# Performance work log

Hardware: AMD Instinct MI355X
Metric: run time of the kernel (lower is better)

The kernel has to match this reference:

```python
import jax, jax.numpy as jnp
import numpy as np

V = 6890  # SMPL vertex count
E = 41328  # directed edges of SMPL mesh
B = 32


def conv1x1(x, W, b):
    # Conv1d kernel=1: pointwise channel mix. x: [B,C,L], W: [O,C], b: [O]
    return jnp.einsum('bcl,oc->bol', x, W) + b[None, :, None]


def setup_inputs() -> dict:
    key = jax.random.key(0)
    ks = jax.random.split(key, 24)
    w = lambda k, s: jax.random.normal(k, s, jnp.float32) * 0.02
    img_feat = jax.random.normal(ks[0], (B, 720, 56, 56), jnp.float32)
    # symmetric random edge list standing in for the fixed SMPL mesh edges
    src = jax.random.randint(ks[1], (E // 2,), 0, V)
    dst = jax.random.randint(ks[2], (E // 2,), 0, V)
    edge_index = jnp.concatenate([jnp.stack([src, dst]), jnp.stack([dst, src])], axis=1).astype(jnp.int32)
    return {
        'img_feat': img_feat,
        'edge_index': edge_index,
        'Wx': w(ks[3], (V, 720)), 'bx': w(ks[4], (V,)),
        'Wy': w(ks[5], (V, 720)), 'by': w(ks[6], (V,)),
        'Wz1': w(ks[7], (56 * 224, 720)), 'bz1': w(ks[8], (56 * 224,)),
        'Wz2': w(ks[9], (V, 224)), 'bz2': w(ks[10], (V,)),
        'Ww1': w(ks[11], (56 * 224, 720)), 'bw1': w(ks[12], (56 * 224,)),
        'Ww2': w(ks[13], (V, 224)), 'bw2': w(ks[14], (V,)),
        'Wg1': w(ks[15], (168, 64)), 'bg1': w(ks[16], (64,)),
        'Wg2': w(ks[17], (64, 32)), 'bg2': w(ks[18], (32,)),
        'Wg3': w(ks[19], (32, 3)), 'bg3': w(ks[20], (3,)),
    }


def reference(img_feat, edge_index, Wx, bx, Wy, by, Wz1, bz1, Wz2, bz2,
              Ww1, bw1, Ww2, bw2, Wg1, bg1, Wg2, bg2, Wg3, bg3):
    b = img_feat.shape[0]
    # 1x1 conv heatmap heads
    heatmap_x = conv1x1(img_feat.mean(2), Wx, bx)            # [B,V,56]
    heatmap_y = conv1x1(img_feat.mean(3), Wy, by)            # [B,V,56]
    feat_g = img_feat.mean((2, 3))[:, :, None]               # [B,720,1]
    heatmap_z = conv1x1(conv1x1(feat_g, Wz1, bz1).reshape(b, 224, 56), Wz2, bz2)
    heatmap_w = conv1x1(conv1x1(feat_g, Ww1, bw1).reshape(b, 224, 56), Ww2, bw2)
    coord_w = jax.nn.sigmoid(heatmap_w.mean(-1, keepdims=True))  # [B,V,1]
    xyz = jnp.concatenate([heatmap_x, heatmap_y, heatmap_z], -1)  # [B,V,168]

    # GCN normalization with self-loops (PyG gcn_norm, edge_weight=1)
    loops = jnp.arange(V, dtype=edge_index.dtype)
    src = jnp.concatenate([edge_index[0], loops])
    dst = jnp.concatenate([edge_index[1], loops])
    deg = jnp.zeros((V,), xyz.dtype).at[dst].add(1.0)
    dinv = jnp.where(deg > 0, jax.lax.rsqrt(deg), 0.0)
    norm = dinv[src] * dinv[dst]                              # [E+V]

    def gcn(x, W, bias):
        xw = x @ W                                            # [B,V,out]
        msg = xw[:, src, :] * norm[None, :, None]             # gather + scale
        agg = jnp.zeros((b, V, W.shape[1]), x.dtype).at[:, dst, :].add(msg)
        return agg + bias

    h = jax.nn.leaky_relu(gcn(xyz, Wg1, bg1))
    h = jax.nn.leaky_relu(gcn(h, Wg2, bg2))
    h = gcn(h, Wg3, bg3)                                      # [B,V,3]
    return jnp.concatenate([h, coord_w], 2)                   # [B,V,4]
```

## Files before the change

### kernel.cpp

```cpp
#include <hip/hip_runtime.h>
#include <hip/hip_bf16.h>
#include <math.h>

#define NV 6890
#define BATCH 32
#define C720 720
#define HW 56
#define K2 1792
#define NBIG 2048
#define MPAD 6912

typedef __attribute__((ext_vector_type(8))) short bf16x8;
typedef __attribute__((ext_vector_type(4))) float f32x4;

__device__ inline void gload16(const void* g, void* l) {
  __builtin_amdgcn_global_load_lds((const __attribute__((address_space(1))) void*)g,
                                   (__attribute__((address_space(3))) void*)l, 16, 0, 0);
}
__device__ inline float bf2f(short s) {
  union { unsigned u; float f; } c; c.u = ((unsigned)(unsigned short)s) << 16; return c.f;
}
__device__ inline short f2bf(float f) {
  __hip_bfloat16 h = (__hip_bfloat16)f; return *(short*)&h;
}

__global__ __launch_bounds__(256) void k_misc(
    const float* __restrict__ Wg1, const float* __restrict__ Ww1, const float* __restrict__ bw1,
    float* __restrict__ S, float* __restrict__ Mw1, float* __restrict__ mb1,
    int* __restrict__ deg) {
  const int blk = blockIdx.x, tid = threadIdx.x;
  if (blk < 672) {
    int c = blk / 3, chunk = blk - c * 3;
    if (tid < 240) {
      int k = chunk * 240 + tid;
      float s = 0.f;
      for (int l = 0; l < HW; ++l) s += Ww1[(size_t)(c * HW + l) * 720 + k];
      Mw1[c * 720 + k] = s * (1.f / HW);
    }
    return;
  }
  if (tid < 64) {
    float s0 = 0, s1 = 0, s2 = 0;
    for (int l = 0; l < HW; ++l) {
      s0 += Wg1[l * 64 + tid];
      s1 += Wg1[(HW + l) * 64 + tid];
      s2 += Wg1[(112 + l) * 64 + tid];
    }
    S[tid] = s0; S[64 + tid] = s1; S[128 + tid] = s2;
  }
  if (tid < 224) {
    float s = 0.f;
    for (int l = 0; l < HW; ++l) s += bw1[tid * HW + l];
    mb1[tid] = s * (1.f / HW);
  }
  for (int v = tid; v < NV; v += 256) deg[v] = 0;
}

__global__ __launch_bounds__(256) void k_deg(const int* __restrict__ ei, int E, int* __restrict__ deg) {
  int e = blockIdx.x * 256 + threadIdx.x;
  if (e < E) atomicAdd(&deg[ei[E + e]], 1);
}

__global__ __launch_bounds__(256) void k_scan(const int* __restrict__ deg,
    int* __restrict__ rowptr, float* __restrict__ dinv, int* __restrict__ cursor) {
  __shared__ int sdata[256];
  const int tid = threadIdx.x;
  const int PER = 27;
  int base = tid * PER, loc[PER], tot = 0;
  #pragma unroll
  for (int i = 0; i < PER; ++i) {
    int idx = base + i;
    int c = (idx < NV) ? deg[idx] + 1 : 0;
    loc[i] = tot; tot += c;
    if (idx < NV) dinv[idx] = rsqrtf((float)c);
  }
  sdata[tid] = tot; __syncthreads();
  for (int off = 1; off < 256; off <<= 1) {
    int v2 = sdata[tid];
    int a = (tid >= off) ? sdata[tid - off] : 0;
    __syncthreads();
    sdata[tid] = v2 + a;
    __syncthreads();
  }
  int excl = sdata[tid] - tot;
  #pragma unroll
  for (int i = 0; i < PER; ++i) {
    int idx = base + i;
    if (idx < NV) { int r = excl + loc[i]; rowptr[idx] = r; cursor[idx] = r; }
  }
  if (tid == 255) rowptr[NV] = sdata[255];
}

__global__ __launch_bounds__(256) void k_fill(const int* __restrict__ ei, int E,
    int* __restrict__ cursor, int* __restrict__ colx) {
  int i = blockIdx.x * 256 + threadIdx.x;
  int N = E + NV;
  if (i >= N) return;
  int s, d;
  if (i < E) { s = ei[i]; d = ei[E + i]; } else { s = d = i - E; }
  colx[atomicAdd(&cursor[d], 1)] = s;
}

__global__ __launch_bounds__(256) void k_wcat(const float* __restrict__ Wx, const float* __restrict__ Wy,
    const float* __restrict__ Wz2, const float* __restrict__ bx, const float* __restrict__ by,
    const float* __restrict__ bz2, __hip_bfloat16* __restrict__ Wcatb) {
  int idx = blockIdx.x * 256 + threadIdx.x;
  int v = idx / 224, c8 = (idx - v * 224) * 8;
  float val[8] = {};
  if (v < NV) {
    const float* s = nullptr;
    if (c8 < 720)                      s = Wx  + (size_t)v * 720 + c8;
    else if (c8 >= 768 && c8 < 1488)   s = Wy  + (size_t)v * 720 + (c8 - 768);
    else if (c8 >= 1536 && c8 < 1760)  s = Wz2 + (size_t)v * 224 + (c8 - 1536);
    if (s) {
      float4 a = *(const float4*)s, b4 = *(const float4*)(s + 4);
      val[0]=a.x; val[1]=a.y; val[2]=a.z; val[3]=a.w;
      val[4]=b4.x; val[5]=b4.y; val[6]=b4.z; val[7]=b4.w;
    } else if (c8 == 1760) {
      val[0] = bx[v]; val[1] = by[v]; val[2] = bz2[v];
    }
  }
  bf16x8 o;
  #pragma unroll
  for (int e = 0; e < 8; ++e) o[e] = f2bf(val[e]);
  *(bf16x8*)(Wcatb + (size_t)v * K2 + c8) = o;
}

__global__ __launch_bounds__(256) void k_imgred(const float* __restrict__ img,
    const float* __restrict__ Wg1, float* __restrict__ P, float* __restrict__ gT) {
  __shared__ float rsumS[64];
  __shared__ float cpartW[4][56];
  __shared__ float csumS[56];
  const int blk = blockIdx.x, tid = threadIdx.x;
  if (blk >= 5760) {
    int r0 = (blk == 5760) ? 720 : 1488;
    float4* dst = (float4*)(P + (size_t)r0 * NBIG);
    for (int i = tid; i < 48 * NBIG / 4; i += 256) dst[i] = (float4){0.f, 0.f, 0.f, 0.f};
    return;
  }
  const int b = blk / C720, c = blk - b * C720;
  const float4* tp4 = (const float4*)(img + (size_t)blk * (HW * HW));
  const int wq = tid & 15, hg = tid >> 4;
  float4 cp = (float4){0.f, 0.f, 0.f, 0.f};
  #pragma unroll
  for (int r = 0; r < 4; ++r) {
    int h = hg + 16 * r;
    bool ok = (wq < 14) & (h < HW);
    float4 v = ok ? tp4[h * 14 + wq] : (float4){0.f, 0.f, 0.f, 0.f};
    cp.x += v.x; cp.y += v.y; cp.z += v.z; cp.w += v.w;
    float rsum = v.x + v.y + v.z + v.w;
    #pragma unroll
    for (int off = 1; off < 16; off <<= 1) rsum += __shfl_xor(rsum, off);
    if (wq == 0 && h < HW) rsumS[h] = rsum;
  }
  #pragma unroll
  for (int off = 16; off < 64; off <<= 1) {
    cp.x += __shfl_xor(cp.x, off); cp.y += __shfl_xor(cp.y, off);
    cp.z += __shfl_xor(cp.z, off); cp.w += __shfl_xor(cp.w, off);
  }
  int wave = tid >> 6, lane = tid & 63;
  if (lane < 14) *(float4*)&cpartW[wave][lane * 4] = cp;
  __syncthreads();
  if (tid < HW) csumS[tid] = cpartW[0][tid] + cpartW[1][tid] + cpartW[2][tid] + cpartW[3][tid];
  __syncthreads();
  if (tid < 64) {
    float ax = 0.f, ay = 0.f;
    #pragma unroll 4
    for (int l = 0; l < HW; ++l) {
      ax += csumS[l] * Wg1[l * 64 + tid];
      ay += rsumS[l] * Wg1[(HW + l) * 64 + tid];
    }
    P[(size_t)c * NBIG + b * 64 + tid] = ax * (1.f / HW);
    P[(size_t)(768 + c) * NBIG + b * 64 + tid] = ay * (1.f / HW);
  } else if (tid < 128) {
    int j = tid - 64;
    float s = (j < HW) ? csumS[j] : 0.f;
    #pragma unroll
    for (int off = 1; off < 64; off <<= 1) s += __shfl_xor(s, off);
    if (j == 0) gT[c * BATCH + b] = s * (1.f / (HW * HW));
  }
}

__global__ __launch_bounds__(256) void k_head1(
    const float* __restrict__ Wz1, const float* __restrict__ bz1,
    const float* __restrict__ gT, float* __restrict__ Z1T) {
  __shared__ float Ws[8 * 720];
  const int blk = blockIdx.x, tid = threadIdx.x;
  const float* src = Wz1 + (size_t)blk * 8 * 720;
  for (int i = tid; i < 1440; i += 256)
    *(float4*)&Ws[i * 4] = *(const float4*)(src + i * 4);
  __syncthreads();
  int rg = tid >> 5, b = tid & 31;
  const float* wr = &Ws[rg * 720];
  float acc = 0.f;
  for (int k = 0; k < C720; k += 4) {
    float4 wv = *(const float4*)(wr + k);
    acc += wv.x * gT[(k    ) * 32 + b];
    acc += wv.y * gT[(k + 1) * 32 + b];
    acc += wv.z * gT[(k + 2) * 32 + b];
    acc += wv.w * gT[(k + 3) * 32 + b];
  }
  int r = blk * 8 + rg;
  Z1T[r * 32 + b] = acc + bz1[r];
}

__global__ __launch_bounds__(256) void k_s3(const float* __restrict__ P,
    const float* __restrict__ Z1T, const float* __restrict__ Mw1, const float* __restrict__ mb1,
    const float* __restrict__ gT,
    const float* __restrict__ Wg1, const float* __restrict__ S,
    __hip_bfloat16* __restrict__ PT, float* __restrict__ w1m) {
  __shared__ float smem[5760];
  const int blk = blockIdx.x, tid = threadIdx.x;
  if (blk < 768) {
    __hip_bfloat16* t = (__hip_bfloat16*)smem;
    int k0 = (blk % 24) * 64, n0 = (blk / 24) * 64;
    int tx = tid & 63, ty4 = tid >> 6;
    #pragma unroll
    for (int i = 0; i < 16; ++i) {
      int k = ty4 * 16 + i;
      t[k * 66 + tx] = (__hip_bfloat16)P[(size_t)(k0 + k) * NBIG + n0 + tx];
    }
    __syncthreads();
    #pragma unroll
    for (int i = 0; i < 16; ++i) {
      int n = ty4 * 16 + i;
      PT[(size_t)(n0 + n) * K2 + k0 + tx] = t[tx * 66 + n];
    }
  } else if (blk < 992) {
    float* Zl = smem;
    float* Wz = smem + 1848;
    const int c = blk - 768;
    for (int i = tid; i < 1792; i += 256) {
      int l = i >> 5, b = i & 31;
      Zl[l * 33 + b] = Z1T[(size_t)c * 1792 + i];
    }
    for (int i = tid; i < 3584; i += 256) Wz[i] = Wg1[112 * 64 + i];
    __syncthreads();
    int n0 = tid * 8, b = n0 >> 6, j0 = n0 & 63;
    float a[8] = {};
    for (int l = 0; l < HW; ++l) {
      float zv = Zl[l * 33 + b];
      const float* wr = &Wz[l * 64 + j0];
      #pragma unroll
      for (int e = 0; e < 8; ++e) a[e] += zv * wr[e];
    }
    #pragma unroll
    for (int e = 0; e < 8; ++e)
      PT[(size_t)(n0 + e) * K2 + 1536 + c] = (__hip_bfloat16)a[e];
  } else if (blk < 1000) {
    int n = (blk - 992) * 256 + tid;
    int j = n & 63;
    bf16x8 o0 = {}, z = {};
    o0[0] = f2bf(S[j]); o0[1] = f2bf(S[64 + j]); o0[2] = f2bf(S[128 + j]);
    __hip_bfloat16* dst = PT + (size_t)n * K2 + 1760;
    *(bf16x8*)dst = o0;
    *(bf16x8*)(dst + 8) = z;
    *(bf16x8*)(dst + 16) = z;
    *(bf16x8*)(dst + 24) = z;
  } else {
    int c0 = (blk - 1000) * 8;
    const float* src = Mw1 + (size_t)c0 * 720;
    for (int i = tid; i < 1440; i += 256)
      *(float4*)&smem[i * 4] = *(const float4*)(src + i * 4);
    __syncthreads();
    int rg = tid >> 5, b = tid & 31;
    const float* wr = &smem[rg * 720];
    float acc = 0.f;
    for (int k = 0; k < C720; k += 4) {
      float4 wv = *(const float4*)(wr + k);
      acc += wv.x * gT[(k    ) * 32 + b];
      acc += wv.y * gT[(k + 1) * 32 + b];
      acc += wv.z * gT[(k + 2) * 32 + b];
      acc += wv.w * gT[(k + 3) * 32 + b];
    }
    int c = c0 + rg;
    w1m[c * 32 + b] = acc + mb1[c];
  }
}

__global__ __launch_bounds__(256) void k_wagg(const __hip_bfloat16* __restrict__ Wcatb,
    const int* __restrict__ rowptr, const int* __restrict__ colx, const float* __restrict__ dinv,
    __hip_bfloat16* __restrict__ Waggb) {
  int w = blockIdx.x * 4 + (threadIdx.x >> 6);
  int lane = threadIdx.x & 63;
  const int i3 = 1536 + lane * 8;
  const bool t3 = i3 < K2;
  __hip_bfloat16* drow = Waggb + (size_t)w * K2;
  if (w >= NV) {
    bf16x8 z = {};
    *(bf16x8*)(drow + lane * 8) = z;
    *(bf16x8*)(drow + 512 + lane * 8) = z;
    *(bf16x8*)(drow + 1024 + lane * 8) = z;
    if (t3) *(bf16x8*)(drow + i3) = z;
    return;
  }
  int r0 = rowptr[w], r1 = rowptr[w + 1];
  float a0[8] = {}, a1[8] = {}, a2[8] = {}, a3[8] = {};
  for (int i = r0; i < r1; ++i) {
    int u = colx[i];
    float wt = dinv[u];
    const __hip_bfloat16* row = Wcatb + (size_t)u * K2;
    bf16x8 x0 = *(const bf16x8*)(row + lane * 8);
    bf16x8 x1 = *(const bf16x8*)(row + 512 + lane * 8);
    bf16x8 x2 = *(const bf16x8*)(row + 1024 + lane * 8);
    #pragma unroll
    for (int e = 0; e < 8; ++e) {
      a0[e] += wt * bf2f(x0[e]);
      a1[e] += wt * bf2f(x1[e]);
      a2[e] += wt * bf2f(x2[e]);
    }
    if (t3) {
      bf16x8 x3 = *(const bf16x8*)(row + i3);
      #pragma unroll
      for (int e = 0; e < 8; ++e) a3[e] += wt * bf2f(x3[e]);
    }
  }
  float dv = dinv[w];
  bf16x8 o0, o1, o2, o3;
  #pragma unroll
  for (int e = 0; e < 8; ++e) {
    o0[e] = f2bf(a0[e] * dv); o1[e] = f2bf(a1[e] * dv);
    o2[e] = f2bf(a2[e] * dv); o3[e] = f2bf(a3[e] * dv);
  }
  *(bf16x8*)(drow + lane * 8) = o0;
  *(bf16x8*)(drow + 512 + lane * 8) = o1;
  *(bf16x8*)(drow + 1024 + lane * 8) = o2;
  if (t3) *(bf16x8*)(drow + i3) = o3;
}

__global__ __launch_bounds__(256) void k_mfma_gemm(
    const __hip_bfloat16* __restrict__ A, const __hip_bfloat16* __restrict__ BT,
    const float* __restrict__ bg1, const float* __restrict__ dinv,
    __hip_bfloat16* __restrict__ p1) {
  __shared__ __hip_bfloat16 As[128 * 64];
  __shared__ __hip_bfloat16 Bs[128 * 64];
  const int tid = threadIdx.x;
  const int wid = tid >> 6, lane = tid & 63;
  const int orig = blockIdx.y * gridDim.x + blockIdx.x;
  const int swz = (orig & 7) * 108 + (orig >> 3);
  const int bxid = swz % (MPAD / 128), byid = swz / (MPAD / 128);
  const int m0 = bxid * 128, n0 = byid * 128;
  const int wr = wid >> 1, wc = wid & 1;
  const int l15 = lane & 15, lhi = lane >> 4;
  const int lk = lhi * 8;

  f32x4 acc[4][4];
  #pragma unroll
  for (int i = 0; i < 4; ++i)
    #pragma unroll
    for (int j = 0; j < 4; ++j) acc[i][j] = (f32x4){0.f, 0.f, 0.f, 0.f};

  const __hip_bfloat16* ag = A  + (size_t)(m0 + (tid >> 3)) * K2 + (tid & 7) * 8;
  const __hip_bfloat16* bg = BT + (size_t)(n0 + (tid >> 3)) * K2 + (tid & 7) * 8;
  const int lbase = wid * 512;

  for (int kt = 0; kt < K2; kt += 64) {
    #pragma unroll
    for (int p = 0; p < 4; ++p) {
      gload16(ag + kt + (size_t)(p * 32) * K2, (void*)&As[p * 2048 + lbase]);
      gload16(bg + kt + (size_t)(p * 32) * K2, (void*)&Bs[p * 2048 + lbase]);
    }
    __syncthreads();
    #pragma unroll
    for (int ks = 0; ks < 2; ++ks) {
      bf16x8 af[4], bf[4];
      #pragma unroll
      for (int mf = 0; mf < 4; ++mf)
        af[mf] = *(const bf16x8*)&As[(wr * 64 + mf * 16 + l15) * 64 + ks * 32 + lk];
      #pragma unroll
      for (int nf = 0; nf < 4; ++nf)
        bf[nf] = *(const bf16x8*)&Bs[(wc * 64 + nf * 16 + l15) * 64 + ks * 32 + lk];
      #pragma unroll
      for (int mf = 0; mf < 4; ++mf)
        #pragma unroll
        for (int nf = 0; nf < 4; ++nf)
          acc[mf][nf] = __builtin_amdgcn_mfma_f32_16x16x32_bf16(af[mf], bf[nf], acc[mf][nf], 0, 0, 0);
    }
    __syncthreads();
  }

  float bgv[4];
  #pragma unroll
  for (int nf = 0; nf < 4; ++nf) bgv[nf] = bg1[nf * 16 + l15];
  #pragma unroll
  for (int mf = 0; mf < 4; ++mf) {
    #pragma unroll
    for (int r = 0; r < 4; ++r) {
      int v = m0 + wr * 64 + mf * 16 + lhi * 4 + r;
      if (v >= NV) continue;
      float dv = dinv[v];
      __hip_bfloat16* pr = p1 + (size_t)v * NBIG + n0 + wc * 64;
      #pragma unroll
      for (int nf = 0; nf < 4; ++nf) {
        int jj = nf * 16 + l15;
        float x = acc[mf][nf][r] + bgv[nf];
        x = x > 0.f ? x : 0.01f * x;
        pr[jj] = (__hip_bfloat16)(x * dv);
      }
    }
  }
}

__global__ __launch_bounds__(256) void k_coordw(const float* __restrict__ Ww2, const float* __restrict__ bw2,
    const float* __restrict__ w1m, float* __restrict__ out) {
  int v = blockIdx.x * 8 + (threadIdx.x >> 5);
  int b = threadIdx.x & 31;
  if (v >= NV) return;
  const float* wr = Ww2 + (size_t)v * 224;
  float acc = 0.f;
  for (int c = 0; c < 224; c += 4) {
    float4 wv = *(const float4*)(wr + c);
    acc += wv.x * w1m[(c    ) * 32 + b];
    acc += wv.y * w1m[(c + 1) * 32 + b];
    acc += wv.z * w1m[(c + 2) * 32 + b];
    acc += wv.w * w1m[(c + 3) * 32 + b];
  }
  acc += bw2[v];
  out[((size_t)b * NV + v) * 4 + 3] = 1.f / (1.f + expf(-acc));
}

__global__ __launch_bounds__(256) void k_t1(const __hip_bfloat16* __restrict__ p1,
    const int* __restrict__ rowptr, const int* __restrict__ colx, const float* __restrict__ dinv,
    const float* __restrict__ Wg2, const float* __restrict__ bg2, __hip_bfloat16* __restrict__ p2) {
  __shared__ float wg[2048];
  __shared__ float g[32 * 66];
  const int v = blockIdx.x, tid = threadIdx.x;
  for (int i = tid; i < 2048; i += 256) wg[i] = Wg2[i];
  const int r0 = rowptr[v], r1 = rowptr[v + 1];
  const int b = tid >> 3, j0 = (tid & 7) * 8;
  float a[8] = {};
  const short* base = (const short*)p1 + tid * 8;
  for (int i = r0; i < r1; ++i) {
    int u = colx[i];
    bf16x8 x = *(const bf16x8*)(base + (size_t)u * NBIG);
    #pragma unroll
    for (int e = 0; e < 8; ++e) a[e] += bf2f(x[e]);
  }
  #pragma unroll
  for (int e = 0; e < 8; e += 2)
    *(float2*)&g[b * 66 + j0 + e] = (float2){a[e], a[e + 1]};
  __syncthreads();
  const float dv = dinv[v];
  const int jg = tid & 7;
  float o0 = 0.f, o1 = 0.f, o2 = 0.f, o3 = 0.f;
  const float* gr = &g[b * 66];
  #pragma unroll 8
  for (int j = 0; j < 64; ++j) {
    float s = gr[j];
    const float* w = &wg[j * 32 + jg];
    o0 += s * w[0]; o1 += s * w[8]; o2 += s * w[16]; o3 += s * w[24];
  }
  __hip_bfloat16* pr = p2 + (size_t)v * 1024 + b * 32 + jg;
  float x0 = o0 * dv + bg2[jg];       x0 = x0 > 0.f ? x0 : 0.01f * x0;
  float x1 = o1 * dv + bg2[jg + 8];   x1 = x1 > 0.f ? x1 : 0.01f * x1;
  float x2 = o2 * dv + bg2[jg + 16];  x2 = x2 > 0.f ? x2 : 0.01f * x2;
  float x3 = o3 * dv + bg2[jg + 24];  x3 = x3 > 0.f ? x3 : 0.01f * x3;
  pr[0]  = (__hip_bfloat16)(x0 * dv);
  pr[8]  = (__hip_bfloat16)(x1 * dv);
  pr[16] = (__hip_bfloat16)(x2 * dv);
  pr[24] = (__hip_bfloat16)(x3 * dv);
}

__global__ __launch_bounds__(128) void k_t2(const __hip_bfloat16* __restrict__ p2,
    const int* __restrict__ rowptr, const int* __restrict__ colx, const float* __restrict__ dinv,
    const float* __restrict__ Wg3, const float* __restrict__ bg3, float* __restrict__ out) {
  __shared__ float wg[96];
  __shared__ float g[32 * 33];
  const int v = blockIdx.x, tid = threadIdx.x;
  if (tid < 96) wg[tid] = Wg3[tid];
  const int r0 = rowptr[v], r1 = rowptr[v + 1];
  const int b = tid >> 2, j0 = (tid & 3) * 8;
  float a[8] = {};
  const short* base = (const short*)p2 + tid * 8;
  for (int i = r0; i < r1; ++i) {
    int u = colx[i];
    bf16x8 x = *(const bf16x8*)(base + (size_t)u * 1024);
    #pragma unroll
    for (int e = 0; e < 8; ++e) a[e] += bf2f(x[e]);
  }
  #pragma unroll
  for (int e = 0; e < 8; ++e) g[b * 33 + j0 + e] = a[e];
  __syncthreads();
  if (tid < 96) {
    int bb = tid & 31, k = tid >> 5;
    float acc = 0.f;
    #pragma unroll 8
    for (int j2 = 0; j2 < 32; ++j2)
      acc += g[bb * 33 + j2] * wg[j2 * 3 + k];
    out[((size_t)bb * NV + v) * 4 + k] = acc * dinv[v] + bg3[k];
  }
}

extern "C" void kernel_launch(void* const* d_in, const int* in_sizes, int n_in,
                              void* d_out, int out_size, void* d_ws, size_t ws_size,
                              hipStream_t stream) {
  const float* img = (const float*)d_in[0];
  const int*   ei  = (const int*)d_in[1];
  const float* Wx  = (const float*)d_in[2];
  const float* bx  = (const float*)d_in[3];
  const float* Wy  = (const float*)d_in[4];
  const float* by  = (const float*)d_in[5];
  const float* Wz1 = (const float*)d_in[6];
  const float* bz1 = (const float*)d_in[7];
  const float* Wz2 = (const float*)d_in[8];
  const float* bz2 = (const float*)d_in[9];
  const float* Ww1 = (const float*)d_in[10];
  const float* bw1 = (const float*)d_in[11];
  const float* Ww2 = (const float*)d_in[12];
  const float* bw2 = (const float*)d_in[13];
  const float* Wg1 = (const float*)d_in[14];
  const float* bg1 = (const float*)d_in[15];
  const float* Wg2 = (const float*)d_in[16];
  const float* bg2 = (const float*)d_in[17];
  const float* Wg3 = (const float*)d_in[18];
  const float* bg3 = (const float*)d_in[19];
  float* out = (float*)d_out;
  int E = in_sizes[1] / 2;

  char* ws = (char*)d_ws;
  __hip_bfloat16* p1     = (__hip_bfloat16*)(ws + 0ULL);
  __hip_bfloat16* p2     = (__hip_bfloat16*)(ws + 28311552ULL);
  __hip_bfloat16* Wcatb  = (__hip_bfloat16*)(ws + 42467328ULL);
  __hip_bfloat16* Waggb  = (__hip_bfloat16*)(ws + 67239936ULL);
  float*          P      = (float*)(ws + 92012544ULL);
  __hip_bfloat16* PT     = (__hip_bfloat16*)(ws + 104595456ULL);
  float*          Z1T    = (float*)(ws + 111935488ULL);
  float*          Mw1    = (float*)(ws + 113541120ULL);
  float*          gT     = (float*)(ws + 114186240ULL);
  float*          w1m    = (float*)(ws + 114278400ULL);
  float*          S      = (float*)(ws + 114307072ULL);
  float*          mb1    = (float*)(ws + 114308096ULL);
  float*          dinv   = (float*)(ws + 114309120ULL);
  int*            rowptr = (int*)(ws + 114336768ULL);
  int*            colx   = (int*)(ws + 114364416ULL);
  int*            deg    = (int*)(ws + 114561024ULL);
  int*            cursor = (int*)(ws + 114588672ULL);

  k_misc<<<673, 256, 0, stream>>>(Wg1, Ww1, bw1, S, Mw1, mb1, deg);
  k_deg<<<(E + 255) / 256, 256, 0, stream>>>(ei, E, deg);
  k_scan<<<1, 256, 0, stream>>>(deg, rowptr, dinv, cursor);
  k_fill<<<(E + NV + 255) / 256, 256, 0, stream>>>(ei, E, cursor, colx);
  k_wcat<<<6048, 256, 0, stream>>>(Wx, Wy, Wz2, bx, by, bz2, Wcatb);
  k_imgred<<<5762, 256, 0, stream>>>(img, Wg1, P, gT);
  k_head1<<<1568, 256, 0, stream>>>(Wz1, bz1, gT, Z1T);
  k_s3<<<1028, 256, 0, stream>>>(P, Z1T, Mw1, mb1, gT, Wg1, S, PT, w1m);
  k_wagg<<<MPAD / 4, 256, 0, stream>>>(Wcatb, rowptr, colx, dinv, Waggb);
  k_mfma_gemm<<<dim3(MPAD / 128, NBIG / 128), 256, 0, stream>>>(Waggb, PT, bg1, dinv, p1);
  k_coordw<<<862, 256, 0, stream>>>(Ww2, bw2, w1m, out);
  k_t1<<<NV, 256, 0, stream>>>(p1, rowptr, colx, dinv, Wg2, bg2, p2);
  k_t2<<<NV, 128, 0, stream>>>(p2, rowptr, colx, dinv, Wg3, bg3, out);
}
```

Measured before the change: 335.0 us.

## Restructure MFMA GEMM into 256x256 tiles with 4-stage async LDS pipeline

The main bf16 GEMM moves from 128x128 tiles with 256 threads and a synchronous load-then-compute loop to 256x256 tiles with 512 threads. It streams K in 32-wide slices through a 4-slot LDS ring, using vmcnt-based waits, XOR-swizzled LDS addressing and raised wave priority around the MFMA bursts. This aims to overlap global loads with compute, cut LDS bank conflicts, and raise data reuse per tile, at the cost of more registers and LDS and only 216 blocks. Separately, the Ww1 mean reduction in k_misc now uses one block per channel group with three columns per thread instead of 672 narrower blocks.

```diff
diff --git a/kernel.cpp b/kernel.cpp
--- a/kernel.cpp
+++ b/kernel.cpp
@@ -9,6 +9,7 @@
 #define K2 1792
 #define NBIG 2048
 #define MPAD 6912
+#define NSLICE 56
 
 typedef __attribute__((ext_vector_type(8))) short bf16x8;
 typedef __attribute__((ext_vector_type(4))) float f32x4;
@@ -29,14 +30,19 @@
     float* __restrict__ S, float* __restrict__ Mw1, float* __restrict__ mb1,
     int* __restrict__ deg) {
   const int blk = blockIdx.x, tid = threadIdx.x;
-  if (blk < 672) {
-    int c = blk / 3, chunk = blk - c * 3;
-    if (tid < 240) {
-      int k = chunk * 240 + tid;
-      float s = 0.f;
-      for (int l = 0; l < HW; ++l) s += Ww1[(size_t)(c * HW + l) * 720 + k];
-      Mw1[c * 720 + k] = s * (1.f / HW);
-    }
+  if (blk < 224) {
+    const float* base = Ww1 + (size_t)blk * HW * 720;
+    float a0 = 0.f, a1 = 0.f, a2 = 0.f;
+    for (int l = 0; l < HW; ++l) {
+      const float* r = base + (size_t)l * 720;
+      a0 += r[tid];
+      a1 += r[tid + 256];
+      if (tid < 208) a2 += r[tid + 512];
+    }
+    float* d = Mw1 + (size_t)blk * 720;
+    d[tid] = a0 * (1.f / HW);
+    d[tid + 256] = a1 * (1.f / HW);
+    if (tid < 208) d[tid + 512] = a2 * (1.f / HW);
     return;
   }
   if (tid < 64) {
@@ -328,74 +334,95 @@
   if (t3) *(bf16x8*)(drow + i3) = o3;
 }
 
-__global__ __launch_bounds__(256) void k_mfma_gemm(
+#define PH_SYNC(N) do { \
+    __builtin_amdgcn_sched_barrier(0); \
+    asm volatile("s_waitcnt vmcnt(" #N ")" ::: "memory"); \
+    __builtin_amdgcn_s_barrier(); \
+    __builtin_amdgcn_sched_barrier(0); } while (0)
+#define PH_END do { \
+    __builtin_amdgcn_sched_barrier(0); \
+    __builtin_amdgcn_s_barrier(); \
+    __builtin_amdgcn_sched_barrier(0); } while (0)
+
+__global__ __launch_bounds__(512) void k_mfma_gemm(
     const __hip_bfloat16* __restrict__ A, const __hip_bfloat16* __restrict__ BT,
     const float* __restrict__ bg1, const float* __restrict__ dinv,
     __hip_bfloat16* __restrict__ p1) {
-  __shared__ __hip_bfloat16 As[128 * 64];
-  __shared__ __hip_bfloat16 Bs[128 * 64];
+  __shared__ __hip_bfloat16 As[4][8192];
+  __shared__ __hip_bfloat16 Bs[4][8192];
   const int tid = threadIdx.x;
   const int wid = tid >> 6, lane = tid & 63;
+  const int wm = wid >> 2, wn = wid & 3;
+  const int l15 = lane & 15, lhi = lane >> 4;
   const int orig = blockIdx.y * gridDim.x + blockIdx.x;
-  const int swz = (orig & 7) * 108 + (orig >> 3);
-  const int bxid = swz % (MPAD / 128), byid = swz / (MPAD / 128);
-  const int m0 = bxid * 128, n0 = byid * 128;
-  const int wr = wid >> 1, wc = wid & 1;
-  const int l15 = lane & 15, lhi = lane >> 4;
-  const int lk = lhi * 8;
-
-  f32x4 acc[4][4];
-  #pragma unroll
-  for (int i = 0; i < 4; ++i)
+  const int swz = (orig & 7) * 27 + (orig >> 3);
+  const int m0 = (swz % 27) * 256, n0 = (swz / 27) * 256;
+
+  const int srow = tid >> 2, o16 = tid & 3;
+  const int k16 = (o16 - srow) & 3;
+  const __hip_bfloat16* agB = A  + (size_t)(m0 + srow) * K2 + k16 * 8;
+  const __hip_bfloat16* bgB = BT + (size_t)(n0 + srow) * K2 + k16 * 8;
+  const size_t rstep = (size_t)128 * K2;
+  const int wbase = wid * 512;
+
+#define STAGE(u) do { int slot_ = (u) & 3; int kt_ = (u) * 32; \
+    gload16(agB + kt_,         (void*)&As[slot_][wbase]); \
+    gload16(agB + kt_ + rstep, (void*)&As[slot_][4096 + wbase]); \
+    gload16(bgB + kt_,         (void*)&Bs[slot_][wbase]); \
+    gload16(bgB + kt_ + rstep, (void*)&Bs[slot_][4096 + wbase]); } while (0)
+
+  f32x4 acc[8][4];
+  #pragma unroll
+  for (int i = 0; i < 8; ++i)
     #pragma unroll
     for (int j = 0; j < 4; ++j) acc[i][j] = (f32x4){0.f, 0.f, 0.f, 0.f};
 
-  const __hip_bfloat16* ag = A  + (size_t)(m0 + (tid >> 3)) * K2 + (tid & 7) * 8;
-  const __hip_bfloat16* bg = BT + (size_t)(n0 + (tid >> 3)) * K2 + (tid & 7) * 8;
-  const int lbase = wid * 512;
-
-  for (int kt = 0; kt < K2; kt += 64) {
-    #pragma unroll
-    for (int p = 0; p < 4; ++p) {
-      gload16(ag + kt + (size_t)(p * 32) * K2, (void*)&As[p * 2048 + lbase]);
-      gload16(bg + kt + (size_t)(p * 32) * K2, (void*)&Bs[p * 2048 + lbase]);
-    }
-    __syncthreads();
-    #pragma unroll
-    for (int ks = 0; ks < 2; ++ks) {
-      bf16x8 af[4], bf[4];
-      #pragma unroll
-      for (int mf = 0; mf < 4; ++mf)
-        af[mf] = *(const bf16x8*)&As[(wr * 64 + mf * 16 + l15) * 64 + ks * 32 + lk];
-      #pragma unroll
-      for (int nf = 0; nf < 4; ++nf)
-        bf[nf] = *(const bf16x8*)&Bs[(wc * 64 + nf * 16 + l15) * 64 + ks * 32 + lk];
-      #pragma unroll
-      for (int mf = 0; mf < 4; ++mf)
-        #pragma unroll
-        for (int nf = 0; nf < 4; ++nf)
-          acc[mf][nf] = __builtin_amdgcn_mfma_f32_16x16x32_bf16(af[mf], bf[nf], acc[mf][nf], 0, 0, 0);
-    }
-    __syncthreads();
-  }
+#define PHASE(slot_) do { \
+    bf16x8 bfr[4]; \
+    _Pragma("unroll") \
+    for (int nf = 0; nf < 4; ++nf) { \
+      int row = wn * 64 + nf * 16 + l15; \
+      bfr[nf] = *(const bf16x8*)&Bs[slot_][row * 32 + ((lhi + row) & 3) * 8]; \
+    } \
+    __builtin_amdgcn_s_setprio(1); \
+    _Pragma("unroll") \
+    for (int mf = 0; mf < 8; ++mf) { \
+      int row = wm * 128 + mf * 16 + l15; \
+      bf16x8 af = *(const bf16x8*)&As[slot_][row * 32 + ((lhi + row) & 3) * 8]; \
+      _Pragma("unroll") \
+      for (int nf = 0; nf < 4; ++nf) \
+        acc[mf][nf] = __builtin_amdgcn_mfma_f32_16x16x32_bf16(af, bfr[nf], acc[mf][nf], 0, 0, 0); \
+    } \
+    __builtin_amdgcn_s_setprio(0); } while (0)
+
+  STAGE(0); STAGE(1); STAGE(2);
+  #pragma unroll 1
+  for (int u = 0; u < NSLICE - 3; ++u) {
+    STAGE(u + 3);
+    PH_SYNC(12);
+    PHASE(u & 3);
+    PH_END;
+  }
+  PH_SYNC(8);  PHASE((NSLICE - 3) & 3); PH_END;
+  PH_SYNC(4);  PHASE((NSLICE - 2) & 3); PH_END;
+  PH_SYNC(0);  PHASE((NSLICE - 1) & 3);
 
   float bgv[4];
   #pragma unroll
   for (int nf = 0; nf < 4; ++nf) bgv[nf] = bg1[nf * 16 + l15];
   #pragma unroll
-  for (int mf = 0; mf < 4; ++mf) {
+  for (int mf = 0; mf < 8; ++mf) {
     #pragma unroll
     for (int r = 0; r < 4; ++r) {
-      int v = m0 + wr * 64 + mf * 16 + lhi * 4 + r;
+      int v = m0 + wm * 128 + mf * 16 + lhi * 4 + r;
       if (v >= NV) continue;
       float dv = dinv[v];
-      __hip_bfloat16* pr = p1 + (size_t)v * NBIG + n0 + wc * 64;
+      __hip_bfloat16* pr = p1 + (size_t)v * NBIG + n0 + wn * 64;
       #pragma unroll
       for (int nf = 0; nf < 4; ++nf) {
-        int jj = nf * 16 + l15;
         float x = acc[mf][nf][r] + bgv[nf];
         x = x > 0.f ? x : 0.01f * x;
-        pr[jj] = (__hip_bfloat16)(x * dv);
+        pr[nf * 16 + l15] = (__hip_bfloat16)(x * dv);
       }
     }
   }
@@ -536,7 +563,7 @@
   int*            deg    = (int*)(ws + 114561024ULL);
   int*            cursor = (int*)(ws + 114588672ULL);
 
-  k_misc<<<673, 256, 0, stream>>>(Wg1, Ww1, bw1, S, Mw1, mb1, deg);
+  k_misc<<<225, 256, 0, stream>>>(Wg1, Ww1, bw1, S, Mw1, mb1, deg);
   k_deg<<<(E + 255) / 256, 256, 0, stream>>>(ei, E, deg);
   k_scan<<<1, 256, 0, stream>>>(deg, rowptr, dinv, cursor);
   k_fill<<<(E + NV + 255) / 256, 256, 0, stream>>>(ei, E, cursor, colx);
@@ -545,7 +572,7 @@
   k_head1<<<1568, 256, 0, stream>>>(Wz1, bz1, gT, Z1T);
   k_s3<<<1028, 256, 0, stream>>>(P, Z1T, Mw1, mb1, gT, Wg1, S, PT, w1m);
   k_wagg<<<MPAD / 4, 256, 0, stream>>>(Wcatb, rowptr, colx, dinv, Waggb);
-  k_mfma_gemm<<<dim3(MPAD / 128, NBIG / 128), 256, 0, stream>>>(Waggb, PT, bg1, dinv, p1);
+  k_mfma_gemm<<<dim3(27, 8), 512, 0, stream>>>(Waggb, PT, bg1, dinv, p1);
   k_coordw<<<862, 256, 0, stream>>>(Ww2, bw2, w1m, out);
   k_t1<<<NV, 256, 0, stream>>>(p1, rowptr, colx, dinv, Wg2, bg2, p2);
   k_t2<<<NV, 128, 0, stream>>>(p2, rowptr, colx, dinv, Wg3, bg3, out);
```

Result: slower. 345.8 us (+3.2%).
